# Kernel optimization log

Measured on AMD Instinct MI355X. Metric: run time of the kernel, lower is better.

## Reference

```python
import math
import jax, jax.numpy as jnp
import numpy as np
from jax import lax

PI = math.pi

def _gauss1d(ks, sigma):
    # kornia gaussian: centered at (ks-1)/2 for both odd and even ks
    x = jnp.arange(ks, dtype=jnp.float32) - (ks - 1) / 2.0
    g = jnp.exp(-0.5 * (x / sigma) ** 2)
    return g / g.sum()

def _unfold_nonoverlap(x, k):
    # F.unfold(x, kernel_size=k, stride=k) for x (B,1,H,W), H,W divisible by k
    B, C, H, W = x.shape
    nH, nW = H // k, W // k
    p = x.reshape(B, nH, k, nW, k).transpose(0, 2, 4, 1, 3)
    return p.reshape(B, k * k, nH * nW)

def _sift(x, ps, nab=8, nsb=4, clipval=0.2, eps=1e-10):
    # kornia SIFTDescriptor(patch_size=ps), x: (N,1,ps,ps) -> (N,128)
    N = x.shape[0]
    g1 = _gauss1d(ps, ps / math.sqrt(2.0))
    gk = jnp.outer(g1, g1)  # (ps,ps), sum 1
    # spatial_gradient mode='diff', normalized, replicate pad
    xp = jnp.pad(x, ((0, 0), (0, 0), (0, 0), (1, 1)), mode='edge')
    gx = 0.5 * (xp[..., 2:] - xp[..., :-2])
    yp = jnp.pad(x, ((0, 0), (0, 0), (1, 1), (0, 0)), mode='edge')
    gy = 0.5 * (yp[:, :, 2:, :] - yp[:, :, :-2, :])
    mag = jnp.sqrt(gx * gx + gy * gy + eps) * gk  # (N,1,ps,ps)
    ori = jnp.arctan2(gy, gx + eps) + 2.0 * PI
    o_big = nab * ori / (2.0 * PI)
    bo0f = jnp.floor(o_big)
    w1 = o_big - bo0f
    bo0 = bo0f.astype(jnp.int32) % nab
    bo1 = (bo0 + 1) % nab
    c0 = jax.nn.one_hot(bo0[:, 0], nab, axis=1, dtype=x.dtype)  # (N,8,ps,ps)
    c1 = jax.nn.one_hot(bo1[:, 0], nab, axis=1, dtype=x.dtype)
    bins = c0 * ((1.0 - w1) * mag) + c1 * (w1 * mag)  # (N,8,ps,ps)
    # triangular pooling kernel, depthwise conv over the 8 angular bins
    bk = 2 * (ps // (nsb + 1)); stride = ps // nsb; pad = bk // 4
    half = bk / 2.0
    xc2 = half - jnp.abs(jnp.arange(bk, dtype=jnp.float32) + 0.5 - half)
    pk = jnp.outer(xc2, xc2) / (half * half)
    pk = jnp.tile(pk[None, None], (nab, 1, 1, 1))  # (8,1,bk,bk)
    pooled = lax.conv_general_dilated(bins, pk, (stride, stride),
        [(pad, pad), (pad, pad)], feature_group_count=nab,
        dimension_numbers=('NCHW', 'OIHW', 'NCHW'))  # (N,8,4,4)
    d = pooled.reshape(N, -1)
    d = d / jnp.maximum(jnp.linalg.norm(d, axis=1, keepdims=True), 1e-12)
    d = jnp.clip(d, 0.0, clipval)
    d = d / jnp.maximum(jnp.linalg.norm(d, axis=1, keepdims=True), 1e-12)
    d = jnp.sqrt(d / jnp.maximum(jnp.abs(d).sum(1, keepdims=True), 1e-12) + eps)  # rootsift
    return d

def _conv_t(x, w, b, stride=2, pad=1):
    # torch ConvTranspose2d; w: (Cin,Cout,k,k)
    k = w.shape[-1]
    wT = jnp.transpose(jnp.flip(w, (-2, -1)), (1, 0, 2, 3))  # (Cout,Cin,k,k)
    y = lax.conv_general_dilated(x, wT, (1, 1),
        [(k - 1 - pad, k - 1 - pad)] * 2, lhs_dilation=(stride, stride),
        dimension_numbers=('NCHW', 'OIHW', 'NCHW'))
    return y + b[None, :, None, None]

def _gn(x, groups, w, b, eps=1e-5):
    N, C, H, W = x.shape
    xg = x.reshape(N, groups, -1)
    mean = xg.mean(-1, keepdims=True)
    var = ((xg - mean) ** 2).mean(-1, keepdims=True)
    xn = ((xg - mean) * lax.rsqrt(var + eps)).reshape(N, C, H, W)
    return xn * w[None, :, None, None] + b[None, :, None, None]

def _jbf(x, guide, ky, kx, sigma_color, sy, sx):
    # kornia joint_bilateral_blur, border='reflect', color_distance='l1'
    B, C, H, W = x.shape
    py, px = ky // 2, kx // 2
    xp = jnp.pad(x, ((0, 0), (0, 0), (py, py), (px, px)), mode='reflect')
    gp = jnp.pad(guide, ((0, 0), (0, 0), (py, py), (px, px)), mode='reflect')
    def win(p):
        return jnp.stack([p[:, :, i:i + H, j:j + W] for i in range(ky) for j in range(kx)], axis=-1)
    ux, ug = win(xp), win(gp)  # (B,C,H,W,ky*kx)
    diff = ug - guide[..., None]
    cd2 = jnp.square(jnp.sum(jnp.abs(diff), axis=1, keepdims=True))
    ck = jnp.exp((-0.5 / (sigma_color ** 2)) * cd2)  # (B,1,H,W,K)
    sk = jnp.outer(_gauss1d(ky, sy), _gauss1d(kx, sx)).reshape(1, 1, 1, 1, -1)
    kern = sk * ck
    return (ux * kern).sum(-1) / kern.sum(-1)

def _forward(x, d1w, d1b, g1w, g1b, s1w, s1b, d2w, d2b, g2w, g2b, s2w, s2b,
             d3w, d3b, g3w, g3b, d4w, d4b, g4w, g4b, fw, fb):
    B = x.shape[0]
    s7 = _sift(_unfold_nonoverlap(x, 7).reshape(-1, 1, 32, 32), 32).reshape(B, 128, 7, 7)
    h = jax.nn.relu(_gn(_conv_t(s7, d1w, d1b), 8, g1w, g1b))  # (B,32,14,14); dropout=identity (eval)
    s14 = _sift(_unfold_nonoverlap(x, 14).reshape(-1, 1, 16, 16), 16).reshape(B, 128, 14, 14)
    sk1 = jnp.einsum('bchw,oc->bohw', s14, s1w[:, :, 0, 0]) + s1b[None, :, None, None]
    h = jax.nn.relu(_gn(_conv_t(jnp.concatenate([h, sk1], 1), d2w, d2b), 4, g2w, g2b))  # (B,16,28,28)
    s28 = _sift(_unfold_nonoverlap(x, 28).reshape(-1, 1, 8, 8), 8).reshape(B, 128, 28, 28)
    sk2 = jnp.einsum('bchw,oc->bohw', s28, s2w[:, :, 0, 0]) + s2b[None, :, None, None]
    h = jax.nn.relu(_gn(_conv_t(jnp.concatenate([h, sk2], 1), d3w, d3b), 2, g3w, g3b))  # (B,8,56,56)
    h = jax.nn.relu(_gn(_conv_t(h, d4w, d4b), 1, g4w, g4b))  # (B,4,112,112)
    h = _conv_t(h, fw, fb)  # (B,2,224,224)
    h = _jbf(h, jnp.tile(x, (1, 2, 1, 1)), 5, 5, 0.1, 1.5, 1.5)
    scale = jnp.array([0.436, 0.615], dtype=h.dtype)
    return jnp.tanh(h) * scale[None, :, None, None]

def setup_inputs() -> dict:
    key = jax.random.key(0)
    ks = jax.random.split(key, 8)
    B = 16
    f32 = jnp.float32
    def rn(k, shp, s=0.05):
        return jax.random.normal(k, shp, f32) * s
    return {
        'x': jax.random.uniform(ks[0], (B, 1, 224, 224), f32),
        'd1w': rn(ks[1], (128, 32, 4, 4)), 'd1b': jnp.zeros((32,), f32),
        'g1w': jnp.ones((32,), f32), 'g1b': jnp.zeros((32,), f32),
        's1w': rn(ks[2], (32, 128, 1, 1)), 's1b': jnp.zeros((32,), f32),
        'd2w': rn(ks[3], (64, 16, 4, 4)), 'd2b': jnp.zeros((16,), f32),
        'g2w': jnp.ones((16,), f32), 'g2b': jnp.zeros((16,), f32),
        's2w': rn(ks[4], (16, 128, 1, 1)), 's2b': jnp.zeros((16,), f32),
        'd3w': rn(ks[5], (32, 8, 4, 4)), 'd3b': jnp.zeros((8,), f32),
        'g3w': jnp.ones((8,), f32), 'g3b': jnp.zeros((8,), f32),
        'd4w': rn(ks[6], (8, 4, 4, 4)), 'd4b': jnp.zeros((4,), f32),
        'g4w': jnp.ones((4,), f32), 'g4b': jnp.zeros((4,), f32),
        'fw': rn(ks[7], (4, 2, 4, 4)), 'fb': jnp.zeros((2,), f32),
    }

def reference(x, d1w, d1b, g1w, g1b, s1w, s1b, d2w, d2b, g2w, g2b, s2w, s2b,
              d3w, d3b, g3w, g3b, d4w, d4b, g4w, g4b, fw, fb):
    return _forward(x, d1w, d1b, g1w, g1b, s1w, s1b, d2w, d2b, g2w, g2b, s2w, s2b,
                    d3w, d3b, g3w, g3b, d4w, d4b, g4w, g4b, fw, fb)
```

## Files before the change

### kernel.cpp

```cpp
#include <hip/hip_runtime.h>
#include <math.h>

#define PI_F 3.14159265358979323846f

template<int PS, int K>
__device__ __forceinline__
void sift_block(const float* __restrict__ x, float* __restrict__ out,
                int n, float* lds)
{
    constexpr int NT = 256;
    constexpr int NPIX = PS*PS;
    constexpr int BK = 2*(PS/5);
    constexpr int STRIDE = PS/4;
    constexpr int PAD = BK/4;
    constexpr float HALF = BK*0.5f;
    constexpr int ROWS = BK/2;

    float* patch = lds;
    float* magp  = patch + NPIX;
    float* obp   = magp + NPIX;
    float* pool2 = obp + NPIX;

    const int tid = threadIdx.x;
    const int b = n / (K*K);
    const int c = n % (K*K);
    const int ki = c / K;
    const int kj = c % K;

    const float* xb = x + (size_t)b*224*224;
    for (int idx = tid; idx < NPIX; idx += NT) {
        int i = idx / PS, j = idx - i*PS;
        patch[idx] = xb[(i*K + ki)*224 + (j*K + kj)];
    }
    __syncthreads();

    const float inv_sig = 1.0f / ((float)PS * 0.70710678118654752440f);
    for (int idx = tid; idx < NPIX; idx += NT) {
        int i = idx / PS, j = idx - i*PS;
        int jm = j > 0 ? j-1 : 0, jp = j < PS-1 ? j+1 : PS-1;
        int im = i > 0 ? i-1 : 0, ip = i < PS-1 ? i+1 : PS-1;
        float gx = 0.5f*(patch[i*PS+jp] - patch[i*PS+jm]);
        float gy = 0.5f*(patch[ip*PS+j] - patch[im*PS+j]);
        float ti = ((float)i - (PS-1)*0.5f) * inv_sig;
        float tj = ((float)j - (PS-1)*0.5f) * inv_sig;
        float wsp = __expf(-0.5f*(ti*ti + tj*tj));
        float mag = sqrtf(gx*gx + gy*gy + 1e-10f) * wsp;
        float ori = atan2f(gy, gx + 1e-10f) + 2.f*PI_F;
        magp[idx] = mag;
        obp[idx]  = ori * (8.f/(2.f*PI_F));
    }
    __syncthreads();

    float pacc = 0.f;
    {
        const int t = tid & 127;
        const int half = tid >> 7;
        const int o = t >> 4;
        const int py = (t >> 2) & 3;
        const int px = t & 3;
        const int sy = py*STRIDE - PAD;
        const int sx = px*STRIDE - PAD;
        for (int dr = 0; dr < ROWS; dr++) {
            int di = half*ROWS + dr;
            int i = sy + di;
            if (i < 0 || i >= PS) continue;
            float wi = HALF - fabsf((float)di + 0.5f - HALF);
            for (int dj = 0; dj < BK; dj++) {
                int j = sx + dj;
                if (j < 0 || j >= PS) continue;
                float wj = HALF - fabsf((float)dj + 0.5f - HALF);
                float m  = magp[i*PS + j];
                float ob = obp[i*PS + j];
                float bo0f = floorf(ob);
                float w1 = ob - bo0f;
                int bo0 = ((int)bo0f) & 7;
                int bo1 = (bo0 + 1) & 7;
                float ctr = (bo0 == o ? (1.f - w1) : 0.f) + (bo1 == o ? w1 : 0.f);
                pacc += ctr * m * (wi*wj);
            }
        }
    }
    pool2[tid] = pacc;
    __syncthreads();

    if (tid < 64) {
        float d0 = pool2[tid]      + pool2[tid + 128];
        float d1 = pool2[tid + 64] + pool2[tid + 192];

        float s = d0*d0 + d1*d1;
        #pragma unroll
        for (int off = 32; off > 0; off >>= 1) s += __shfl_xor(s, off);
        float nrm = fmaxf(sqrtf(s), 1e-12f);
        d0 /= nrm; d1 /= nrm;
        d0 = fminf(fmaxf(d0, 0.f), 0.2f);
        d1 = fminf(fmaxf(d1, 0.f), 0.2f);
        s = d0*d0 + d1*d1;
        #pragma unroll
        for (int off = 32; off > 0; off >>= 1) s += __shfl_xor(s, off);
        nrm = fmaxf(sqrtf(s), 1e-12f);
        d0 /= nrm; d1 /= nrm;
        s = d0 + d1;
        #pragma unroll
        for (int off = 32; off > 0; off >>= 1) s += __shfl_xor(s, off);
        s = fmaxf(s, 1e-12f);
        d0 = sqrtf(d0/s + 1e-10f);
        d1 = sqrtf(d1/s + 1e-10f);

        out[(size_t)n*128 + tid]      = d0;
        out[(size_t)n*128 + 64 + tid] = d1;
    }
}

__device__ __forceinline__
void sift8_block(const float* __restrict__ x, float* __restrict__ out, int bid)
{
    const int tid = threadIdx.x;
    const int l = tid & 63;
    const int wv = tid >> 6;
    const int n = bid*4 + wv;
    const int b = n / 784;
    const int c = n % 784;
    const int ki = c / 28, kj = c % 28;
    const int i = l >> 3, j = l & 7;

    const float* xb = x + (size_t)b*50176;
    float v = xb[(i*28 + ki)*224 + (j*28 + kj)];

    int lL = (j > 0) ? l-1 : l;
    int lR = (j < 7) ? l+1 : l;
    int lU = (i > 0) ? l-8 : l;
    int lD = (i < 7) ? l+8 : l;
    float pL = __shfl(v, lL);
    float pR = __shfl(v, lR);
    float pU = __shfl(v, lU);
    float pD = __shfl(v, lD);
    float gx = 0.5f*(pR - pL);
    float gy = 0.5f*(pD - pU);

    float ti = ((float)i - 3.5f) * (1.f/5.65685424949238f);
    float tj = ((float)j - 3.5f) * (1.f/5.65685424949238f);
    float wsp = __expf(-0.5f*(ti*ti + tj*tj));
    float mag = sqrtf(gx*gx + gy*gy + 1e-10f) * wsp;
    float ori = atan2f(gy, gx + 1e-10f) + 2.f*PI_F;
    float obig = ori * (8.f/(2.f*PI_F));
    float bo0f = floorf(obig);
    float w1 = obig - bo0f;
    int bo0 = ((int)bo0f) & 7;
    int bo1 = (bo0 + 1) & 7;
    float c0 = (1.f - w1)*mag;
    float c1 = w1*mag;

    const int t = ((i & 1) << 1) | (j & 1);
    float d0 = 0.f, d1 = 0.f;
    #pragma unroll
    for (int o = 0; o < 8; o++) {
        float val = (bo0 == o ? c0 : 0.f) + (bo1 == o ? c1 : 0.f);
        val += __shfl_xor(val, 1);
        val += __shfl_xor(val, 8);
        if (o == 2*t)     d0 = val;
        if (o == 2*t + 1) d1 = val;
    }

    float s = d0*d0 + d1*d1;
    #pragma unroll
    for (int off = 32; off > 0; off >>= 1) s += __shfl_xor(s, off);
    float nrm = fmaxf(sqrtf(s), 1e-12f);
    d0 /= nrm; d1 /= nrm;
    d0 = fminf(fmaxf(d0, 0.f), 0.2f);
    d1 = fminf(fmaxf(d1, 0.f), 0.2f);
    s = d0*d0 + d1*d1;
    #pragma unroll
    for (int off = 32; off > 0; off >>= 1) s += __shfl_xor(s, off);
    nrm = fmaxf(sqrtf(s), 1e-12f);
    d0 /= nrm; d1 /= nrm;
    s = d0 + d1;
    #pragma unroll
    for (int off = 32; off > 0; off >>= 1) s += __shfl_xor(s, off);
    s = fmaxf(s, 1e-12f);
    d0 = sqrtf(d0/s + 1e-10f);
    d1 = sqrtf(d1/s + 1e-10f);

    int cell = (i >> 1)*4 + (j >> 1);
    float* ob = out + (size_t)n*128 + cell;
    ob[(2*t)*16]     = d0;
    ob[(2*t + 1)*16] = d1;
}

__global__ __launch_bounds__(256)
void sift_all(const float* __restrict__ x, float* __restrict__ s7,
              float* __restrict__ s14, float* __restrict__ s28)
{
    __shared__ float lds[3328];
    const int bid = blockIdx.x;
    if (bid < 784) {
        sift_block<32, 7>(x, s7, bid, lds);
    } else if (bid < 3920) {
        sift_block<16, 14>(x, s14, bid - 784, lds);
    } else {
        sift8_block(x, s28, bid - 3920);
    }
}

template<int CO, int S>
__device__ __forceinline__
void conv1x1_block(const float* __restrict__ in, const float* __restrict__ w,
                   const float* __restrict__ bias, float* __restrict__ out,
                   int bid, float* wt)
{
    const int tid = threadIdx.x;
    for (int i = tid; i < 128*CO; i += 256) {
        int c = i / CO, co = i - c*CO;
        wt[i] = w[co*128 + c];
    }
    __syncthreads();
    int idx = bid*256 + tid;
    int s = idx % S; int r = idx / S;
    int co4 = r % (CO/4); int b = r / (CO/4);
    int co = co4*4;
    const float* ib = in + (size_t)b*128*S + s;
    float acc0 = bias[co], acc1 = bias[co+1], acc2 = bias[co+2], acc3 = bias[co+3];
    #pragma unroll 8
    for (int c = 0; c < 128; c++) {
        float v = ib[c*S];
        const float4 wv = *(const float4*)&wt[c*CO + co];
        acc0 += v*wv.x; acc1 += v*wv.y; acc2 += v*wv.z; acc3 += v*wv.w;
    }
    float* ob = out + ((size_t)b*CO + co)*S + s;
    ob[0] = acc0; ob[S] = acc1; ob[2*S] = acc2; ob[3*S] = acc3;
}

__device__ __forceinline__
void convt_l1_block(const float* __restrict__ in0, const float* __restrict__ w,
                    const float* __restrict__ bias,
                    float* __restrict__ out, float2* __restrict__ pst_out,
                    int by, float* lds)
{
    constexpr int CIN = 128, COUT = 32, HIN = 7, NCH = 4, NT = 256;
    constexpr int H0 = 14, SP = 196, HIN2 = 49;
    constexpr int NR = 9, WIN = 9, TILE = CIN*NR*WIN;
    constexpr int WSTRIDE = CIN*NCH*4 + 4;

    float* tile  = lds;
    float* wl2   = tile + TILE;
    float* wpart = wl2 + 4*WSTRIDE;

    const int tid = threadIdx.x;
    const int b  = by >> 3;
    const int cb = by & 7;
    const int c0 = cb*NCH;

    for (int idx = tid; idx < 4*CIN*NCH*4; idx += NT) {
        int k = idx & 3;
        int t2 = idx >> 2;
        int j = t2 % NCH; t2 /= NCH;
        int ci = t2 % CIN;
        int pq = t2 / CIN;
        int pA = pq >> 1, qA = pq & 1;
        int dy = pA + 2*(k>>1), dx = qA + 2*(k&1);
        wl2[pq*WSTRIDE + (ci*NCH + j)*4 + k] = w[(ci*COUT + c0 + j)*16 + dy*4 + dx];
    }
    const float* i0 = in0 + (size_t)b*CIN*HIN2;
    for (int idx = tid; idx < TILE; idx += NT) {
        int c = idx % WIN;
        int t2 = idx / WIN;
        int r = t2 % NR;
        int ci = t2 / NR;
        int iy = r - 1, ix = c - 1;
        float v = 0.f;
        if (iy >= 0 && iy < HIN && ix >= 0 && ix < HIN)
            v = i0[ci*HIN2 + iy*HIN + ix];
        tile[idx] = v;
    }
    __syncthreads();

    float acc[NCH];
    #pragma unroll
    for (int j = 0; j < NCH; j++) acc[j] = 0.f;

    const bool active = tid < SP;
    if (active) {
        int oy = tid / H0, ox = tid % H0;
        int pA = (oy+1)&1, qA = (ox+1)&1;
        int iyA = (oy+1-pA)>>1, ixA = (ox+1-qA)>>1;
        int toff = (iyA+1)*WIN + (ixA+1);
        const float* wbase = wl2 + (pA*2+qA)*WSTRIDE;

        #pragma unroll
        for (int j = 0; j < NCH; j++) acc[j] = bias[c0 + j];

        #pragma unroll 4
        for (int ci = 0; ci < CIN; ci++) {
            const float* tp = tile + ci*(NR*WIN) + toff;
            float l0 = tp[0];
            float l1 = tp[-1];
            float l2 = tp[-WIN];
            float l3 = tp[-WIN-1];
            const float* wr = wbase + ci*NCH*4;
            #pragma unroll
            for (int j = 0; j < NCH; j++) {
                const float4 wv = *(const float4*)(wr + j*4);
                acc[j] += l0*wv.x + l1*wv.y + l2*wv.z + l3*wv.w;
            }
        }
        float* ob = out + ((size_t)b*COUT + c0)*SP + tid;
        #pragma unroll
        for (int j = 0; j < NCH; j++) ob[j*SP] = acc[j];
    }

    const int wv = tid >> 6;
    const int ln = tid & 63;
    float ps = 0.f, pq2 = 0.f;
    #pragma unroll
    for (int j = 0; j < NCH; j++) {
        float v = active ? acc[j] : 0.f;
        ps += v; pq2 += v*v;
    }
    #pragma unroll
    for (int off = 32; off > 0; off >>= 1) {
        ps  += __shfl_down(ps,  off);
        pq2 += __shfl_down(pq2, off);
    }
    if (ln == 0) { wpart[wv*2] = ps; wpart[wv*2+1] = pq2; }
    __syncthreads();
    if (tid == 0) {
        float s0 = wpart[0]+wpart[2]+wpart[4]+wpart[6];
        float s1 = wpart[1]+wpart[3]+wpart[5]+wpart[7];
        pst_out[(size_t)b*8 + cb] = make_float2(s0, s1);
    }
}

__global__ __launch_bounds__(256)
void skip_l1(const float* __restrict__ s14, const float* __restrict__ s28,
             const float* __restrict__ s1w, const float* __restrict__ s1b,
             const float* __restrict__ s2w, const float* __restrict__ s2b,
             const float* __restrict__ s7,  const float* __restrict__ d1w,
             const float* __restrict__ d1b,
             float* __restrict__ sk1, float* __restrict__ sk2,
             float* __restrict__ h1, float2* __restrict__ pst1)
{
    __shared__ float lds[18584];
    const int bid = blockIdx.x;
    if (bid < 98)       conv1x1_block<32, 196>(s14, s1w, s1b, sk1, bid, lds);
    else if (bid < 294) conv1x1_block<16, 784>(s28, s2w, s2b, sk2, bid - 98, lds);
    else                convt_l1_block(s7, d1w, d1b, h1, pst1, bid - 294, lds);
}

template<int CIN0, int CIN1, int COUT, int G, int HIN, int NCH, int RT, int NT,
         bool FUSE, int GIN, int NGIN, int NBLK_IN, int NBLK_OUT>
__global__ __launch_bounds__(NT)
void convt_tiled(const float* __restrict__ in0, const float* __restrict__ in1,
                 const float* __restrict__ w, const float* __restrict__ bias,
                 const float2* __restrict__ pst_in,
                 const float* __restrict__ gnw, const float* __restrict__ gnb,
                 float* __restrict__ out, float2* __restrict__ pst_out)
{
    constexpr int CIN = CIN0 + CIN1;
    constexpr int CG = COUT / G;
    constexpr int NGRP = NCH / CG;
    constexpr int CB = COUT / NCH;
    constexpr int H0 = 2*HIN;
    constexpr int SP = H0*H0;
    constexpr int HIN2 = HIN*HIN;
    constexpr int NR = RT/2 + 2;
    constexpr int WIN = HIN + 2;
    constexpr int TILE = CIN*NR*WIN;
    constexpr int WSTRIDE = CIN*NCH*4 + 4;
    constexpr int NPOS = RT*H0;
    constexpr int NWAVE = NT/64;

    __shared__ float tile[TILE];
    __shared__ float wl2[4*WSTRIDE];
    __shared__ float a_s[CIN0];
    __shared__ float b_s[CIN0];
    __shared__ float wpart[NWAVE][NGRP][2];

    const int tid = threadIdx.x;
    const int by = blockIdx.y;
    const int bx = blockIdx.x;
    const int b  = by / CB;
    const int cb = by - b*CB;
    const int c0 = cb*NCH;
    const int g0 = c0 / CG;
    const int r0 = bx * RT;
    const int row0 = r0/2 - 1;

    if constexpr (FUSE) {
        if (tid < CIN0) {
            int gi = tid / (CIN0/GIN);
            float s0 = 0.f, s1 = 0.f;
            for (int k = 0; k < NBLK_IN; k++) {
                float2 p = pst_in[((size_t)b*GIN + gi)*NBLK_IN + k];
                s0 += p.x; s1 += p.y;
            }
            float mean = s0 * (1.f/NGIN);
            float var  = s1 * (1.f/NGIN) - mean*mean;
            float inv  = rsqrtf(var + 1e-5f);
            float a = inv * gnw[tid];
            a_s[tid] = a;
            b_s[tid] = gnb[tid] - mean*a;
        }
        __syncthreads();
    }

    for (int idx = tid; idx < 4*CIN*NCH*4; idx += NT) {
        int k = idx & 3;
        int t2 = idx >> 2;
        int j = t2 % NCH; t2 /= NCH;
        int ci = t2 % CIN;
        int pq = t2 / CIN;
        int pA = pq >> 1, qA = pq & 1;
        int dy = pA + 2*(k>>1), dx = qA + 2*(k&1);
        wl2[pq*WSTRIDE + (ci*NCH + j)*4 + k] = w[(ci*COUT + c0 + j)*16 + dy*4 + dx];
    }

    const float* i0 = in0 + (size_t)b*CIN0*HIN2;
    for (int idx = tid; idx < TILE; idx += NT) {
        int c = idx % WIN;
        int t2 = idx / WIN;
        int r = t2 % NR;
        int ci = t2 / NR;
        int iy = row0 + r, ix = c - 1;
        float v = 0.f;
        if (iy >= 0 && iy < HIN && ix >= 0 && ix < HIN) {
            if (CIN1 == 0 || ci < CIN0) {
                v = i0[ci*HIN2 + iy*HIN + ix];
                if constexpr (FUSE) v = fmaxf(v*a_s[ci] + b_s[ci], 0.f);
            } else {
                v = in1[((size_t)b*CIN1 + (ci-CIN0))*HIN2 + iy*HIN + ix];
            }
        }
        tile[idx] = v;
    }
    __syncthreads();

    float acc[NCH];
    #pragma unroll
    for (int j = 0; j < NCH; j++) acc[j] = 0.f;

    const bool active = tid < NPOS;
    if (active) {
        int oy = r0 + tid / H0, ox = tid % H0;
        int pA = (oy+1)&1, qA = (ox+1)&1;
        int iyA = (oy+1-pA)>>1, ixA = (ox+1-qA)>>1;
        int rA = iyA - row0;
        int cA = ixA + 1;
        int toff = rA*WIN + cA;
        const float* wbase = wl2 + (pA*2+qA)*WSTRIDE;

        #pragma unroll
        for (int j = 0; j < NCH; j++) acc[j] = bias[c0 + j];

        #pragma unroll 4
        for (int ci = 0; ci < CIN; ci++) {
            const float* tp = tile + ci*(NR*WIN) + toff;
            float l0 = tp[0];
            float l1 = tp[-1];
            float l2 = tp[-WIN];
            float l3 = tp[-WIN-1];
            const float* wr = wbase + ci*NCH*4;
            #pragma unroll
            for (int j = 0; j < NCH; j++) {
                const float4 wv = *(const float4*)(wr + j*4);
                acc[j] += l0*wv.x + l1*wv.y + l2*wv.z + l3*wv.w;
            }
        }
        float* ob = out + ((size_t)b*COUT + c0)*SP + r0*H0 + tid;
        #pragma unroll
        for (int j = 0; j < NCH; j++) ob[j*SP] = acc[j];
    }

    const int wv = tid >> 6;
    const int ln = tid & 63;
    #pragma unroll
    for (int grp = 0; grp < NGRP; grp++) {
        float ps = 0.f, pq2 = 0.f;
        #pragma unroll
        for (int j = 0; j < CG; j++) {
            float v = active ? acc[grp*CG + j] : 0.f;
            ps += v; pq2 += v*v;
        }
        #pragma unroll
        for (int off = 32; off > 0; off >>= 1) {
            ps  += __shfl_down(ps,  off);
            pq2 += __shfl_down(pq2, off);
        }
        if (ln == 0) { wpart[wv][grp][0] = ps; wpart[wv][grp][1] = pq2; }
    }
    __syncthreads();
    if (tid < NGRP) {
        float s0 = 0.f, s1 = 0.f;
        #pragma unroll
        for (int w2 = 0; w2 < NWAVE; w2++) { s0 += wpart[w2][tid][0]; s1 += wpart[w2][tid][1]; }
        pst_out[((size_t)b*G + g0 + tid)*NBLK_OUT + bx] = make_float2(s0, s1);
    }
}

__global__ __launch_bounds__(256)
void final_bilateral(const float* __restrict__ h4, const float* __restrict__ fw,
                     const float* __restrict__ fb, const float2* __restrict__ pst_in,
                     const float* __restrict__ gnw, const float* __restrict__ gnb,
                     const float* __restrict__ x, float* __restrict__ out)
{
    const float g[5] = {0.1200783f, 0.2338817f, 0.2920800f, 0.2338817f, 0.1200783f};
    __shared__ float xs[400], p0s[400], p1s[400];
    __shared__ float wl2[128];
    __shared__ float a_s[4], b_s[4], bl[2], mv[2];

    const int tid = threadIdx.x;
    const int b = blockIdx.z;
    const int ty0 = blockIdx.y*16;
    const int tx0 = blockIdx.x*16;
    const float* xb = x + (size_t)b*50176;

    if (tid < 128) {
        int k = tid & 3;
        int t = tid >> 2;
        int co = t & 1; t >>= 1;
        int ci = t & 3;
        int pq = t >> 2;
        int pA = pq >> 1, qA = pq & 1;
        int dy = pA + 2*(k>>1), dx = qA + 2*(k&1);
        wl2[tid] = fw[(ci*2 + co)*16 + dy*4 + dx];
    }
    if (tid < 2) bl[tid] = fb[tid];
    if (tid >= 192) {
        int k0 = tid - 192;
        float s0 = 0.f, s1 = 0.f;
        if (k0 < 56) {
            float2 p = pst_in[(size_t)b*56 + k0];
            s0 = p.x; s1 = p.y;
        }
        #pragma unroll
        for (int off = 32; off > 0; off >>= 1) {
            s0 += __shfl_down(s0, off);
            s1 += __shfl_down(s1, off);
        }
        if (k0 == 0) {
            float mean = s0 * (1.f/50176.f);
            float var  = s1 * (1.f/50176.f) - mean*mean;
            mv[0] = mean;
            mv[1] = rsqrtf(var + 1e-5f);
        }
    }
    __syncthreads();
    if (tid < 4) {
        float a = mv[1] * gnw[tid];
        a_s[tid] = a;
        b_s[tid] = gnb[tid] - mv[0]*a;
    }
    __syncthreads();

    const float* ib = h4 + (size_t)b*4*12544;
    for (int idx = tid; idx < 400; idx += 256) {
        int r = idx / 20, cc = idx - r*20;
        int oy = ty0 - 2 + r;  oy = oy < 0 ? -oy : (oy > 223 ? 446 - oy : oy);
        int ox = tx0 - 2 + cc; ox = ox < 0 ? -ox : (ox > 223 ? 446 - ox : ox);
        xs[idx] = xb[oy*224 + ox];

        int pA = (oy+1)&1, iyA = (oy+1-pA)>>1, iyB = iyA-1;
        int qA = (ox+1)&1, ixA = (ox+1-qA)>>1, ixB = ixA-1;
        float mYA = (iyA < 112) ? 1.f : 0.f;
        float mYB = (iyB >= 0)  ? 1.f : 0.f;
        float mXA = (ixA < 112) ? 1.f : 0.f;
        float mXB = (ixB >= 0)  ? 1.f : 0.f;
        float m0 = mYA*mXA, m1 = mYA*mXB, m2 = mYB*mXA, m3 = mYB*mXB;
        int iyAc = min(iyA, 111), iyBc = max(iyB, 0);
        int ixAc = min(ixA, 111), ixBc = max(ixB, 0);
        int oAA = iyAc*112 + ixAc, oAB = iyAc*112 + ixBc;
        int oBA = iyBc*112 + ixAc, oBB = iyBc*112 + ixBc;
        const float* wbase = wl2 + (pA*2+qA)*32;

        float acc0 = bl[0], acc1 = bl[1];
        #pragma unroll
        for (int ci = 0; ci < 4; ci++) {
            const float* ip = ib + ci*12544;
            float a = a_s[ci], bb = b_s[ci];
            float l0 = fmaxf(ip[oAA]*a + bb, 0.f);
            float l1 = fmaxf(ip[oAB]*a + bb, 0.f);
            float l2 = fmaxf(ip[oBA]*a + bb, 0.f);
            float l3 = fmaxf(ip[oBB]*a + bb, 0.f);
            float t0 = l0*m0, t1 = l1*m1, t2 = l2*m2, t3 = l3*m3;
            const float4 w0 = *(const float4*)(wbase + ci*8);
            const float4 w1 = *(const float4*)(wbase + ci*8 + 4);
            acc0 += t0*w0.x + t1*w0.y + t2*w0.z + t3*w0.w;
            acc1 += t0*w1.x + t1*w1.y + t2*w1.z + t3*w1.w;
        }
        p0s[idx] = acc0;
        p1s[idx] = acc1;
    }
    __syncthreads();

    int ly = tid >> 4, lx = tid & 15;
    int base = (ly+2)*20 + (lx+2);
    float center = xs[base];
    float wsum = 0.f, a0 = 0.f, a1 = 0.f;
    #pragma unroll
    for (int di = -2; di <= 2; di++){
        #pragma unroll
        for (int dj = -2; dj <= 2; dj++){
            int o = base + di*20 + dj;
            float dg = xs[o] - center;
            float wgt = g[di+2]*g[dj+2]*__expf(-200.f*dg*dg);
            wsum += wgt;
            a0 += wgt * p0s[o];
            a1 += wgt * p1s[o];
        }
    }
    float inv = 1.0f / wsum;
    int s = (ty0 + ly)*224 + (tx0 + lx);
    out[(size_t)(b*2)*50176 + s]     = tanhf(a0*inv)*0.436f;
    out[(size_t)(b*2+1)*50176 + s]   = tanhf(a1*inv)*0.615f;
}

extern "C" void kernel_launch(void* const* d_in, const int* in_sizes, int n_in,
                              void* d_out, int out_size, void* d_ws, size_t ws_size,
                              hipStream_t stream) {
    (void)in_sizes; (void)n_in; (void)out_size; (void)ws_size;
    const float* x   = (const float*)d_in[0];
    const float* d1w = (const float*)d_in[1];
    const float* d1b = (const float*)d_in[2];
    const float* g1w = (const float*)d_in[3];
    const float* g1b = (const float*)d_in[4];
    const float* s1w = (const float*)d_in[5];
    const float* s1b = (const float*)d_in[6];
    const float* d2w = (const float*)d_in[7];
    const float* d2b = (const float*)d_in[8];
    const float* g2w = (const float*)d_in[9];
    const float* g2b = (const float*)d_in[10];
    const float* s2w = (const float*)d_in[11];
    const float* s2b = (const float*)d_in[12];
    const float* d3w = (const float*)d_in[13];
    const float* d3b = (const float*)d_in[14];
    const float* g3w = (const float*)d_in[15];
    const float* g3b = (const float*)d_in[16];
    const float* d4w = (const float*)d_in[17];
    const float* d4b = (const float*)d_in[18];
    const float* g4w = (const float*)d_in[19];
    const float* g4b = (const float*)d_in[20];
    const float* fw  = (const float*)d_in[21];
    const float* fb  = (const float*)d_in[22];
    float* out = (float*)d_out;

    float* ws  = (float*)d_ws;
    float* s7  = ws;
    float* s14 = s7  + 100352;
    float* s28 = s14 + 401408;
    float* sk1 = s28 + 1605632;
    float* sk2 = sk1 + 100352;
    float* h1  = sk2 + 200704;
    float* h2  = h1  + 100352;
    float* h3  = h2  + 200704;
    float* h4  = h3  + 401408;
    float2* pst1 = (float2*)(h4 + 802816);
    float2* pst2 = pst1 + 128;
    float2* pst3 = pst2 + 448;
    float2* pst4 = pst3 + 448;

    sift_all<<<7056, 256, 0, stream>>>(x, s7, s14, s28);

    skip_l1<<<422, 256, 0, stream>>>(s14, s28, s1w, s1b, s2w, s2b,
                                     s7, d1w, d1b, sk1, sk2, h1, pst1);

    convt_tiled< 32,32, 16, 4, 14, 8,  4, 128, true, 8, 784, 1, 7>
        <<<dim3(7, 16*2), 128, 0, stream>>>(h1, sk1, d2w, d2b, pst1, g1w, g1b, h2, pst2);
    convt_tiled< 16,16,  8, 2, 28, 8,  4, 256, true, 4, 3136, 7, 14>
        <<<dim3(14, 16), 256, 0, stream>>>(h2, sk2, d3w, d3b, pst2, g2w, g2b, h3, pst3);
    convt_tiled<  8, 0,  4, 1, 56, 4,  2, 256, true, 2, 12544, 14, 56>
        <<<dim3(56, 16), 256, 0, stream>>>(h3, nullptr, d4w, d4b, pst3, g3w, g3b, h4, pst4);

    final_bilateral<<<dim3(14, 14, 16), 256, 0, stream>>>(h4, fw, fb, pst4, g4w, g4b, x, out);
}
```

Measured before the change: 226.2 us.

## Precompute SIFT bin weights, pool all 8 bins per thread, coalesce weight loads

The SIFT pooling stage now precomputes each pixel's two bin contributions and its bin index once, instead of recomputing floor and bin logic for every orientation thread. Each group of 16 threads accumulates all 8 orientation bins over one spatial window and reduces them with shuffles, which removes the 8x redundant tap traversal. Transposed-conv weight staging now iterates over the contiguous source tap, giving coalesced global reads, and the first convt launch moves from 128 to 256 threads. The cost is more LDS per SIFT block (which may reduce occupancy) and extra register pressure from the 8 accumulators.

```diff
diff --git a/kernel.cpp b/kernel.cpp
--- a/kernel.cpp
+++ b/kernel.cpp
@@ -14,12 +14,12 @@
     constexpr int STRIDE = PS/4;
     constexpr int PAD = BK/4;
     constexpr float HALF = BK*0.5f;
-    constexpr int ROWS = BK/2;
 
     float* patch = lds;
-    float* magp  = patch + NPIX;
-    float* obp   = magp + NPIX;
-    float* pool2 = obp + NPIX;
+    float* c0p   = patch + NPIX;
+    float* c1p   = c0p + NPIX;
+    float* bo0p  = c1p + NPIX;
+    float* pool2 = bo0p + NPIX;
 
     const int tid = threadIdx.x;
     const int b = n / (K*K);
@@ -46,46 +46,59 @@
         float wsp = __expf(-0.5f*(ti*ti + tj*tj));
         float mag = sqrtf(gx*gx + gy*gy + 1e-10f) * wsp;
         float ori = atan2f(gy, gx + 1e-10f) + 2.f*PI_F;
-        magp[idx] = mag;
-        obp[idx]  = ori * (8.f/(2.f*PI_F));
-    }
-    __syncthreads();
-
-    float pacc = 0.f;
+        float ob  = ori * (8.f/(2.f*PI_F));
+        float bo0f = floorf(ob);
+        float w1 = ob - bo0f;
+        int bo0 = ((int)bo0f) & 7;
+        c0p[idx]  = (1.f - w1)*mag;
+        c1p[idx]  = w1*mag;
+        bo0p[idx] = (float)bo0;
+    }
+    __syncthreads();
+
     {
-        const int t = tid & 127;
-        const int half = tid >> 7;
-        const int o = t >> 4;
-        const int py = (t >> 2) & 3;
-        const int px = t & 3;
+        const int win = tid >> 4;
+        const int sub = tid & 15;
+        const int py = win >> 2;
+        const int px = win & 3;
         const int sy = py*STRIDE - PAD;
         const int sx = px*STRIDE - PAD;
-        for (int dr = 0; dr < ROWS; dr++) {
-            int di = half*ROWS + dr;
-            int i = sy + di;
-            if (i < 0 || i >= PS) continue;
-            float wi = HALF - fabsf((float)di + 0.5f - HALF);
-            for (int dj = 0; dj < BK; dj++) {
-                int j = sx + dj;
-                if (j < 0 || j >= PS) continue;
-                float wj = HALF - fabsf((float)dj + 0.5f - HALF);
-                float m  = magp[i*PS + j];
-                float ob = obp[i*PS + j];
-                float bo0f = floorf(ob);
-                float w1 = ob - bo0f;
-                int bo0 = ((int)bo0f) & 7;
-                int bo1 = (bo0 + 1) & 7;
-                float ctr = (bo0 == o ? (1.f - w1) : 0.f) + (bo1 == o ? w1 : 0.f);
-                pacc += ctr * m * (wi*wj);
+        float acc[8];
+        #pragma unroll
+        for (int o = 0; o < 8; o++) acc[o] = 0.f;
+
+        for (int tap = sub; tap < BK*BK; tap += 16) {
+            int di = tap / BK, dj = tap - di*BK;
+            int i = sy + di, j = sx + dj;
+            if (i < 0 || i >= PS || j < 0 || j >= PS) continue;
+            float wgt = (HALF - fabsf((float)di + 0.5f - HALF)) *
+                        (HALF - fabsf((float)dj + 0.5f - HALF));
+            int idx = i*PS + j;
+            float c0 = c0p[idx] * wgt;
+            float c1 = c1p[idx] * wgt;
+            float bo = bo0p[idx];
+            #pragma unroll
+            for (int o = 0; o < 8; o++) {
+                float ctr = (bo == (float)o) ? c0 :
+                            ((bo == (float)((o+7)&7)) ? c1 : 0.f);
+                acc[o] += ctr;
             }
         }
-    }
-    pool2[tid] = pacc;
+        #pragma unroll
+        for (int o = 0; o < 8; o++) {
+            float v = acc[o];
+            v += __shfl_xor(v, 1);
+            v += __shfl_xor(v, 2);
+            v += __shfl_xor(v, 4);
+            v += __shfl_xor(v, 8);
+            if (sub == 0) pool2[o*16 + win] = v;
+        }
+    }
     __syncthreads();
 
     if (tid < 64) {
-        float d0 = pool2[tid]      + pool2[tid + 128];
-        float d1 = pool2[tid + 64] + pool2[tid + 192];
+        float d0 = pool2[tid];
+        float d1 = pool2[tid + 64];
 
         float s = d0*d0 + d1*d1;
         #pragma unroll
@@ -190,7 +203,7 @@
 void sift_all(const float* __restrict__ x, float* __restrict__ s7,
               float* __restrict__ s14, float* __restrict__ s28)
 {
-    __shared__ float lds[3328];
+    __shared__ float lds[4224];
     const int bid = blockIdx.x;
     if (bid < 784) {
         sift_block<32, 7>(x, s7, bid, lds);
@@ -249,15 +262,15 @@
     const int cb = by & 7;
     const int c0 = cb*NCH;
 
-    for (int idx = tid; idx < 4*CIN*NCH*4; idx += NT) {
-        int k = idx & 3;
-        int t2 = idx >> 2;
-        int j = t2 % NCH; t2 /= NCH;
-        int ci = t2 % CIN;
-        int pq = t2 / CIN;
-        int pA = pq >> 1, qA = pq & 1;
-        int dy = pA + 2*(k>>1), dx = qA + 2*(k&1);
-        wl2[pq*WSTRIDE + (ci*NCH + j)*4 + k] = w[(ci*COUT + c0 + j)*16 + dy*4 + dx];
+    for (int idx = tid; idx < CIN*NCH*16; idx += NT) {
+        int tap = idx & 15;
+        int t2 = idx >> 4;
+        int j = t2 % NCH;
+        int ci = t2 / NCH;
+        int dy = tap >> 2, dx = tap & 3;
+        int pq = (dy & 1)*2 + (dx & 1);
+        int k  = (dy >> 1)*2 + (dx >> 1);
+        wl2[pq*WSTRIDE + (ci*NCH + j)*4 + k] = w[(ci*COUT + c0 + j)*16 + tap];
     }
     const float* i0 = in0 + (size_t)b*CIN*HIN2;
     for (int idx = tid; idx < TILE; idx += NT) {
@@ -402,15 +415,15 @@
         __syncthreads();
     }
 
-    for (int idx = tid; idx < 4*CIN*NCH*4; idx += NT) {
-        int k = idx & 3;
-        int t2 = idx >> 2;
-        int j = t2 % NCH; t2 /= NCH;
-        int ci = t2 % CIN;
-        int pq = t2 / CIN;
-        int pA = pq >> 1, qA = pq & 1;
-        int dy = pA + 2*(k>>1), dx = qA + 2*(k&1);
-        wl2[pq*WSTRIDE + (ci*NCH + j)*4 + k] = w[(ci*COUT + c0 + j)*16 + dy*4 + dx];
+    for (int idx = tid; idx < CIN*NCH*16; idx += NT) {
+        int tap = idx & 15;
+        int t2 = idx >> 4;
+        int j = t2 % NCH;
+        int ci = t2 / NCH;
+        int dy = tap >> 2, dx = tap & 3;
+        int pq = (dy & 1)*2 + (dx & 1);
+        int k  = (dy >> 1)*2 + (dx >> 1);
+        wl2[pq*WSTRIDE + (ci*NCH + j)*4 + k] = w[(ci*COUT + c0 + j)*16 + tap];
     }
 
     const float* i0 = in0 + (size_t)b*CIN0*HIN2;
@@ -661,8 +674,8 @@
     skip_l1<<<422, 256, 0, stream>>>(s14, s28, s1w, s1b, s2w, s2b,
                                      s7, d1w, d1b, sk1, sk2, h1, pst1);
 
-    convt_tiled< 32,32, 16, 4, 14, 8,  4, 128, true, 8, 784, 1, 7>
-        <<<dim3(7, 16*2), 128, 0, stream>>>(h1, sk1, d2w, d2b, pst1, g1w, g1b, h2, pst2);
+    convt_tiled< 32,32, 16, 4, 14, 8,  4, 256, true, 8, 784, 1, 7>
+        <<<dim3(7, 16*2), 256, 0, stream>>>(h1, sk1, d2w, d2b, pst1, g1w, g1b, h2, pst2);
     convt_tiled< 16,16,  8, 2, 28, 8,  4, 256, true, 4, 3136, 7, 14>
         <<<dim3(14, 16), 256, 0, stream>>>(h2, sk2, d3w, d3b, pst2, g2w, g2b, h3, pst3);
     convt_tiled<  8, 0,  4, 1, 56, 4,  2, 256, true, 2, 12544, 14, 56>
```

New measurement: 217.5 us, median of 2. -3.9%, faster.
